# Optimization experiments

Measured on AMD Instinct MI355X. Metric: run time of the kernel, lower is better.

## Reference

```python
import jax, jax.numpy as jnp
import numpy as np
jax.config.update("jax_enable_x64", True)

TAPS, DELAY = 5, 3
EPS = 1e-6        # DNN_WPE.eps: power clamp before WPE
WPE_EPS = 1e-10   # wpe_one_iteration eps: inverse-power clamp + diag loading


def _signal_framing(Y, L):
    # Y: (..., T) -> (..., T-L+1, L) sliding frames (as_strided equivalent)
    T = Y.shape[-1]
    idx = jnp.arange(T - L + 1)[:, None] + jnp.arange(L)[None, :]
    return Y[..., idx]


def _wpe_one_iteration(Y, power, taps, delay):
    # Y: (B,F,C,T) complex128, power: (B,F,T) float64
    B, F, C, T = Y.shape
    inv_power = 1.0 / jnp.maximum(power, WPE_EPS)
    Tp = T - delay - taps + 1
    # tap-stacked delayed signal, taps axis reversed: (B,F,C,Tp,taps)
    Psi = _signal_framing(Y, taps)[..., :Tp, :][..., ::-1]
    Psi_n = Psi.conj() * inv_power[:, :, None, delay + taps - 1:, None]
    # covariance R: (B,F,taps*C,taps*C); cross-corr P: (B,F,taps,C_e,C_d)
    R = jnp.einsum("bfdtk,bfetl->bfkdle", Psi_n, Psi).reshape(B, F, taps * C, taps * C)
    P = jnp.einsum("bfdtk,bfet->bfked", Psi_n, Y[..., delay + taps - 1:])
    # v: (B,F,C_e,taps*C_d); conj filter G = inv(R) @ v^T  (X = v @ inv(R)^T)
    v = P.transpose(0, 1, 3, 2, 4).reshape(B, F, C, taps * C)
    eye = jnp.eye(taps * C, dtype=R.dtype)
    tr = jnp.trace(R, axis1=-2, axis2=-1).real[..., None, None] / (taps * C)
    G = jnp.linalg.solve(R + WPE_EPS * tr * eye, v.transpose(0, 1, 3, 2))
    G = G.reshape(B, F, taps, C, C)  # (B,F,tau,d,e) conjugated filter matrix
    # reverb tail: sum over taps of filtered, delayed signal
    tail = jnp.zeros_like(Y)
    for tau in range(taps):  # taps=5, small fixed loop
        s = delay + tau
        contrib = jnp.einsum("bfde,bfdt->bfet", G[:, :, tau], Y[..., : T - s])
        tail = tail.at[..., s:].add(contrib)
    return Y - tail


def setup_inputs() -> dict:
    key = jax.random.key(0)
    k1, k2, k3 = jax.random.split(key, 3)
    B, T, C, F = 4, 512, 8, 257
    data_real = jax.random.normal(k1, (B, T, C, F), dtype=jnp.float32)
    data_imag = jax.random.normal(k2, (B, T, C, F), dtype=jnp.float32)
    ilens = jax.random.randint(k3, (B,), 256, T + 1)
    return {"data_real": data_real, "data_imag": data_imag, "ilens": ilens}


def reference(data_real, data_imag, ilens):
    # (B,T,C,F) -> (B,F,C,T)
    data = (data_real + 1j * data_imag).transpose(0, 3, 2, 1)
    # power averaged over channels, clamped (B,F,T)
    power = jnp.maximum(jnp.mean(data.real ** 2 + data.imag ** 2, axis=-2), EPS)
    enh = _wpe_one_iteration(data.astype(jnp.complex128), power.astype(jnp.float64), TAPS, DELAY)
    enh = enh.astype(jnp.complex64)
    T = enh.shape[-1]
    pad = (jnp.arange(T)[None, :] >= ilens[:, None])[:, None, None, :]  # (B,1,1,T)
    enh = jnp.where(pad, 0.0 + 0.0j, enh)
    enh = enh.transpose(0, 3, 2, 1)  # back to (B,T,C,F)
    return enh.real, enh.imag, power
```

## Files before the change

### kernel.cpp

```cpp
#include <hip/hip_runtime.h>
#include <hip/hip_fp16.h>

#define B_ 4
#define T_ 512
#define C_ 8
#define F_ 257
#define TAPS 5
#define DELAY 3
#define N_ 40
#define NA 48
#define TP 505
#define T0 7
#define BF (B_*F_)
#define BTCF ((size_t)B_*T_*C_*F_)
#define YSH 532
#define YPAD 8
#define ZSD 20

typedef _Float16 half8 __attribute__((ext_vector_type(8)));
typedef float floatx4 __attribute__((ext_vector_type(4)));
typedef uint32_t uint32x4 __attribute__((ext_vector_type(4)));

__device__ inline uint32_t h2mul(uint32_t a, uint32_t b) {
    __half2 r = __hmul2(__builtin_bit_cast(__half2, a), __builtin_bit_cast(__half2, b));
    return __builtin_bit_cast(uint32_t, r);
}
__device__ inline uint32_t packf16(float2 v) {
    __half2 h = __floats2half2_rn(v.x, v.y);
    return __builtin_bit_cast(uint32_t, h);
}
__device__ inline float2 unpackf16(uint32_t u) {
    __half2 h = __builtin_bit_cast(__half2, u);
    return make_float2(__low2float(h), __high2float(h));
}
__device__ inline half8 mkfrag(uint32_t a, uint32_t b, uint32_t c, uint32_t d) {
    uint32x4 v = {a, b, c, d};
    return __builtin_bit_cast(half8, v);
}
__device__ inline int rowoff(int i) {
    return i * 49 - ((i * (i - 1)) >> 1);
}

struct Frag { half8 X; half8 Y; };

__device__ inline Frag build2(const uint32_t* p, uint32_t sw0, uint32_t sw1,
                              uint32_t sw2, uint32_t sw3) {
    uint32_t q0 = p[0], q1 = p[1], q2 = p[2], q3 = p[3];
    uint32_t q4 = p[4], q5 = p[5], q6 = p[6], q7 = p[7];
    uint32_t x0 = __builtin_amdgcn_perm(q1, q0, 0x05040100);
    uint32_t y0 = __builtin_amdgcn_perm(q1, q0, 0x07060302);
    uint32_t x1 = __builtin_amdgcn_perm(q3, q2, 0x05040100);
    uint32_t y1 = __builtin_amdgcn_perm(q3, q2, 0x07060302);
    uint32_t x2 = __builtin_amdgcn_perm(q5, q4, 0x05040100);
    uint32_t y2 = __builtin_amdgcn_perm(q5, q4, 0x07060302);
    uint32_t x3 = __builtin_amdgcn_perm(q7, q6, 0x05040100);
    uint32_t y3 = __builtin_amdgcn_perm(q7, q6, 0x07060302);
    Frag f;
    f.X = mkfrag(h2mul(x0, sw0), h2mul(x1, sw1), h2mul(x2, sw2), h2mul(x3, sw3));
    f.Y = mkfrag(h2mul(y0, sw0), h2mul(y1, sw1), h2mul(y2, sw2), h2mul(y3, sw3));
    return f;
}
__device__ inline int zs_off(int j) {
    return (j < N_) ? (j & 7) * YSH + (YPAD + 4 - (j >> 3)) : (j - N_) * YSH + (YPAD + T0);
}

__global__ __launch_bounds__(256) void k_fused(const float* __restrict__ in_re,
                                               const float* __restrict__ in_im,
                                               const int* __restrict__ ilens,
                                               float* __restrict__ out_re,
                                               float* __restrict__ out_im,
                                               float* __restrict__ pow_out) {
    __shared__ uint32_t sYh[C_ * YSH];
    __shared__ __align__(16) uint32_t pool[3256];
    float* sPow = (float*)pool;
    float2* sGT = (float2*)pool;
    uint32_t* sw_pk = pool + 640;
    float2* sAugU = (float2*)(pool + 896);
    int tid = threadIdx.x;

    int bid = blockIdx.x;
    int xcd = bid & 7, slot = bid >> 3;
    int w = (xcd < 4) ? xcd * 129 + slot : 516 + (xcd - 4) * 128 + slot;
    int b = w / F_;
    int f = w - b * F_;
    int ilen = ilens[b];
    const float* pre = in_re + (size_t)b * T_ * C_ * F_ + f;
    const float* pim = in_im + (size_t)b * T_ * C_ * F_ + f;

    {
        int t0 = tid, t1 = tid + 256;
        float s0 = 0.f, s1 = 0.f;
#pragma unroll 4
        for (int c = 0; c < C_; ++c) {
            size_t a0 = ((size_t)t0 * C_ + c) * F_;
            size_t a1 = ((size_t)t1 * C_ + c) * F_;
            float xr0 = pre[a0], xi0 = pim[a0];
            float xr1 = pre[a1], xi1 = pim[a1];
            sYh[c * YSH + YPAD + t0] = packf16(make_float2(xr0, xi0));
            sYh[c * YSH + YPAD + t1] = packf16(make_float2(xr1, xi1));
            s0 += xr0 * xr0 + xi0 * xi0;
            s1 += xr1 * xr1 + xi1 * xi1;
        }
        if (tid < 20) {
            int z = (tid < 8) ? tid : (512 + tid);
#pragma unroll
            for (int c = 0; c < C_; ++c) sYh[c * YSH + z] = 0;
        }
        s0 = fmaxf(s0 * (1.0f / C_), 1e-6f);
        s1 = fmaxf(s1 * (1.0f / C_), 1e-6f);
        pow_out[(size_t)w * T_ + t0] = s0;
        pow_out[(size_t)w * T_ + t1] = s1;
        sPow[t0] = s0;
        sPow[t1] = s1;
    }
    __syncthreads();

    {
        int k0 = 2 * tid, k1 = k0 + 1;
        float w0 = (k0 < TP) ? rsqrtf(sPow[k0 + T0]) : 0.f;
        float w1 = (k1 < TP) ? rsqrtf(sPow[k1 + T0]) : 0.f;
        sw_pk[tid] = packf16(make_float2(w0, w1));
    }
    __syncthreads();

    int wv = tid >> 6, ln = tid & 63;
    int kg = ln >> 4;
    if (wv < 3) {
        int r16 = ln & 15;
        int offB = zs_off(wv * 16 + r16);
#pragma unroll 1
        for (int mt = 0; mt < 3; ++mt) {
            int offA = zs_off(mt * 16 + r16);
            floatx4 aRe = {0.f, 0.f, 0.f, 0.f};
            floatx4 aIm = {0.f, 0.f, 0.f, 0.f};
#pragma unroll 2
            for (int ks = 0; ks < 16; ++ks) {
                int kbase = ks * 32 + kg * 8;
                uint32x4 sv = *(const uint32x4*)&sw_pk[kbase >> 1];
                Frag B = build2(&sYh[offB + kbase], sv[0], sv[1], sv[2], sv[3]);
                Frag A = build2(&sYh[offA + kbase], sv[0], sv[1], sv[2], sv[3]);
                half8 nYa = -A.Y;
                aRe = __builtin_amdgcn_mfma_f32_16x16x32_f16(A.X, B.X, aRe, 0, 0, 0);
                aRe = __builtin_amdgcn_mfma_f32_16x16x32_f16(A.Y, B.Y, aRe, 0, 0, 0);
                aIm = __builtin_amdgcn_mfma_f32_16x16x32_f16(A.X, B.Y, aIm, 0, 0, 0);
                aIm = __builtin_amdgcn_mfma_f32_16x16x32_f16(nYa, B.X, aIm, 0, 0, 0);
            }
#pragma unroll
            for (int r = 0; r < 4; ++r) {
                int m = mt * 16 + kg * 4 + r;
                int col = wv * 16 + r16;
                if (m < N_ && col >= m)
                    sAugU[rowoff(m) + col - m] = make_float2(aRe[r], aIm[r]);
            }
        }
    }
    __syncthreads();

    if (tid < 64) {
        float dv = (tid < N_) ? sAugU[rowoff(tid)].x : 0.f;
#pragma unroll
        for (int off = 32; off; off >>= 1) dv += __shfl_xor(dv, off, 64);
        if (tid < N_) sAugU[rowoff(tid)].x += 1e-10f * dv / N_;
    }
    __syncthreads();

    {
        int ri = tid >> 4, ci = tid & 15;
        float2 dq0, dq1, dq2;
#pragma unroll 1
        for (int p = 0; p < N_ - 2; p += 2) {
            if (p > 0 && ri == 0) {
                int qm = p - 1, roqm = rowoff(qm);
                if (ci < NA - qm)      sAugU[roqm + ci] = dq0;
                if (ci + 16 < NA - qm) sAugU[roqm + ci + 16] = dq1;
                if (ci + 32 < NA - qm) sAugU[roqm + ci + 32] = dq2;
            }
            int q = p + 1;
            int rop = rowoff(p), roq = rowoff(q);
            float2 Upp = sAugU[rop];
            float2 Upq = sAugU[rop + 1];
            float2 Uqq = sAugU[roq];
            float dn0 = Upp.x * Upp.x + Upp.y * Upp.y;
            float i0x = Upp.x / dn0, i0y = -Upp.y / dn0;
            float mqx = Upq.x * i0x + Upq.y * i0y;
            float mqy = Upq.x * i0y - Upq.y * i0x;
            float d1x = Uqq.x - (mqx * Upq.x - mqy * Upq.y);
            float d1y = Uqq.y - (mqx * Upq.y + mqy * Upq.x);
            float dn1 = d1x * d1x + d1y * d1y;
            float i1x = d1x / dn1, i1y = -d1y / dn1;
#pragma unroll 1
            for (int i = q + ri; i < N_; i += 16) {
                if (i == q) {
#pragma unroll
                    for (int s = 0; s < 3; ++s) {
                        int j = q + ci + 16 * s;
                        float2 r = make_float2(0.f, 0.f);
                        if (j < NA) {
                            float2 Upj = sAugU[rop + j - p];
                            float2 Uqj = sAugU[roq + j - q];
                            r.x = Uqj.x - (mqx * Upj.x - mqy * Upj.y);
                            r.y = Uqj.y - (mqx * Upj.y + mqy * Upj.x);
                        }
                        if (s == 0) dq0 = r; else if (s == 1) dq1 = r; else dq2 = r;
                    }
                } else {
                    float2 Upi = sAugU[rop + i - p];
                    float m0x = Upi.x * i0x + Upi.y * i0y;
                    float m0y = Upi.x * i0y - Upi.y * i0x;
                    float2 Uqi = sAugU[roq + i - q];
                    float ax = Uqi.x - (m0x * Upq.x - m0y * Upq.y);
                    float ay = -Uqi.y - (m0x * Upq.y + m0y * Upq.x);
                    float m1x = ax * i1x - ay * i1y;
                    float m1y = ax * i1y + ay * i1x;
                    int roi = rowoff(i) - i;
#pragma unroll 1
                    for (int j = i + ci; j < NA; j += 16) {
                        float2 Upj = sAugU[rop + j - p];
                        float2 Uqj = sAugU[roq + j - q];
                        float u1x = Uqj.x - (mqx * Upj.x - mqy * Upj.y);
                        float u1y = Uqj.y - (mqx * Upj.y + mqy * Upj.x);
                        float2 v = sAugU[roi + j];
                        v.x -= (m0x * Upj.x - m0y * Upj.y) + (m1x * u1x - m1y * u1y);
                        v.y -= (m0x * Upj.y + m0y * Upj.x) + (m1x * u1y + m1y * u1x);
                        sAugU[roi + j] = v;
                    }
                }
            }
            __syncthreads();
        }
        {
            int p = N_ - 2;
            if (ri == 0) {
                int qm = p - 1, roqm = rowoff(qm);
                if (ci < NA - qm)      sAugU[roqm + ci] = dq0;
                if (ci + 16 < NA - qm) sAugU[roqm + ci + 16] = dq1;
                if (ci + 32 < NA - qm) sAugU[roqm + ci + 32] = dq2;
            }
            int rop = rowoff(p);
            float2 piv = sAugU[rop];
            float dn = piv.x * piv.x + piv.y * piv.y;
            float px = piv.x / dn, py = -piv.y / dn;
#pragma unroll 1
            for (int i = p + 1 + ri; i < N_; i += 16) {
                float2 api = sAugU[rop + i - p];
                float mx = api.x * px + api.y * py;
                float my = api.x * py - api.y * px;
                int roi = rowoff(i) - i;
#pragma unroll 1
                for (int j = i + ci; j < NA; j += 16) {
                    float2 apj = sAugU[rop + j - p];
                    float2 v = sAugU[roi + j];
                    v.x -= mx * apj.x - my * apj.y;
                    v.y -= mx * apj.y + my * apj.x;
                    sAugU[roi + j] = v;
                }
            }
            __syncthreads();
        }
    }
    {
        int bc = tid & 7, br = tid >> 3;
        float2 defv = make_float2(0.f, 0.f);
        int defRow = -1;
#pragma unroll 1
        for (int p = N_ - 1; p >= 3; p -= 2) {
            if (defRow >= 0 && br == (defRow & 31))
                sAugU[rowoff(defRow) + N_ + bc - defRow] = defv;
            int q = p - 1;
            int rop = rowoff(p), roq = rowoff(q);
            float2 pivP = sAugU[rop];
            float dnP = pivP.x * pivP.x + pivP.y * pivP.y;
            float pPx = pivP.x / dnP, pPy = -pivP.y / dnP;
            float2 rhsP = sAugU[rop + N_ + bc - p];
            float xPx = rhsP.x * pPx - rhsP.y * pPy;
            float xPy = rhsP.x * pPy + rhsP.y * pPx;
            float2 pivQ = sAugU[roq];
            float dnQ = pivQ.x * pivQ.x + pivQ.y * pivQ.y;
            float pQx = pivQ.x / dnQ, pQy = -pivQ.y / dnQ;
            float2 Uqp = sAugU[roq + 1];
            float2 rhsQ = sAugU[roq + N_ + bc - q];
            float rqx = rhsQ.x - (Uqp.x * xPx - Uqp.y * xPy);
            float rqy = rhsQ.y - (Uqp.x * xPy + Uqp.y * xPx);
            float xQx = rqx * pQx - rqy * pQy;
            float xQy = rqx * pQy + rqy * pQx;
#pragma unroll 1
            for (int i = br; i <= p - 2; i += 32) {
                int roi = rowoff(i) - i;
                float2 Uip = sAugU[roi + p];
                float2 Uiq = sAugU[roi + q];
                float2 v = sAugU[roi + N_ + bc];
                v.x -= (Uip.x * xPx - Uip.y * xPy) + (Uiq.x * xQx - Uiq.y * xQy);
                v.y -= (Uip.x * xPy + Uip.y * xPx) + (Uiq.x * xQy + Uiq.y * xQx);
                sAugU[roi + N_ + bc] = v;
            }
            if (br == (q & 31)) defv = make_float2(rqx, rqy);
            defRow = q;
            __syncthreads();
        }
        {
            if (defRow >= 0 && br == (defRow & 31))
                sAugU[rowoff(defRow) + N_ + bc - defRow] = defv;
            int rop = rowoff(1);
            float2 piv = sAugU[rop];
            float dn = piv.x * piv.x + piv.y * piv.y;
            float px = piv.x / dn, py = -piv.y / dn;
            float2 rhs = sAugU[rop + N_ + bc - 1];
            float xr = rhs.x * px - rhs.y * py;
            float xi = rhs.x * py + rhs.y * px;
            if (br == 0) {
                float2 aip = sAugU[1];
                float2 v = sAugU[N_ + bc];
                v.x -= aip.x * xr - aip.y * xi;
                v.y -= aip.x * xi + aip.y * xr;
                sAugU[N_ + bc] = v;
            }
            __syncthreads();
        }
    }
    for (int idx = tid; idx < N_ * C_; idx += 256) {
        int j = idx >> 3;
        int e = idx & 7;
        int roj = rowoff(j);
        float2 piv = sAugU[roj];
        float dnm = piv.x * piv.x + piv.y * piv.y;
        float pix = piv.x / dnm, piy = -piv.y / dnm;
        float2 rhs = sAugU[roj + N_ + e - j];
        int tau = j >> 3, d = j & 7;
        sGT[(e * C_ + d) * TAPS + tau] =
            make_float2(rhs.x * pix - rhs.y * piy, rhs.x * piy + rhs.y * pix);
    }
    __syncthreads();

    half8 aFr[2], aFi[2];
    {
        int m = ln & 15;
#pragma unroll
        for (int ks = 0; ks < 2; ++ks) {
            half8 hr = {}, hi = {};
#pragma unroll
            for (int q = 0; q < 8; ++q) {
                int j = ks * 32 + kg * 8 + q;
                float gx = 0.f, gy = 0.f;
                if (m < 8 && j < N_) {
                    float2 g = sGT[(m * C_ + (j & 7)) * TAPS + (j >> 3)];
                    gx = g.x; gy = g.y;
                }
                hr[q] = (_Float16)gx;
                hi[q] = (_Float16)gy;
            }
            aFr[ks] = hr;
            aFi[ks] = hi;
        }
    }
    __syncthreads();

    uint32_t* zRe = pool;
    uint32_t* zIm = pool + 64 * ZSD;
    int trow = wv * 16 + (ln & 15);
#pragma unroll 1
    for (int ch = 0; ch < 8; ++ch) {
        int c0 = ch * 64;
        for (int idx = tid; idx < 1280; idx += 256) {
            int jp = idx >> 6, tl = idx & 63;
            int j0 = 2 * jp, j1 = j0 + 1;
            int base = c0 + tl + (YPAD - 3);
            uint32_t y0 = sYh[(j0 & 7) * YSH + base - (j0 >> 3)];
            uint32_t y1 = sYh[(j1 & 7) * YSH + base - (j1 >> 3)];
            zRe[tl * ZSD + jp] = __builtin_amdgcn_perm(y1, y0, 0x05040100);
            zIm[tl * ZSD + jp] = __builtin_amdgcn_perm(y1, y0, 0x07060302);
        }
        __syncthreads();
        floatx4 accR = {0.f, 0.f, 0.f, 0.f};
        floatx4 accI = {0.f, 0.f, 0.f, 0.f};
        {
            int o0 = trow * ZSD + kg * 4;
            half8 Br0 = __builtin_bit_cast(half8, *(const uint32x4*)&zRe[o0]);
            half8 Bi0 = __builtin_bit_cast(half8, *(const uint32x4*)&zIm[o0]);
            half8 Br1 = {}, Bi1 = {};
            if (kg == 0) {
                int o1 = trow * ZSD + 16;
                Br1 = __builtin_bit_cast(half8, *(const uint32x4*)&zRe[o1]);
                Bi1 = __builtin_bit_cast(half8, *(const uint32x4*)&zIm[o1]);
            }
            half8 nFi0 = -aFi[0], nFi1 = -aFi[1];
            accR = __builtin_amdgcn_mfma_f32_16x16x32_f16(aFr[0], Br0, accR, 0, 0, 0);
            accR = __builtin_amdgcn_mfma_f32_16x16x32_f16(aFr[1], Br1, accR, 0, 0, 0);
            accI = __builtin_amdgcn_mfma_f32_16x16x32_f16(aFi[0], Br0, accI, 0, 0, 0);
            accI = __builtin_amdgcn_mfma_f32_16x16x32_f16(aFi[1], Br1, accI, 0, 0, 0);
            accR = __builtin_amdgcn_mfma_f32_16x16x32_f16(nFi0, Bi0, accR, 0, 0, 0);
            accR = __builtin_amdgcn_mfma_f32_16x16x32_f16(nFi1, Bi1, accR, 0, 0, 0);
            accI = __builtin_amdgcn_mfma_f32_16x16x32_f16(aFr[0], Bi0, accI, 0, 0, 0);
            accI = __builtin_amdgcn_mfma_f32_16x16x32_f16(aFr[1], Bi1, accI, 0, 0, 0);
        }
        if (kg < 2) {
            int tg = c0 + trow;
            bool dead = (tg >= ilen);
#pragma unroll
            for (int r = 0; r < 4; ++r) {
                int e = kg * 4 + r;
                float2 cf = unpackf16(sYh[e * YSH + YPAD + tg]);
                float ex = cf.x - accR[r];
                float ey = cf.y - accI[r];
                if (dead) { ex = 0.f; ey = 0.f; }
                size_t o = (size_t)b * T_ * C_ * F_ + ((size_t)tg * C_ + e) * F_ + f;
                out_re[o] = ex;
                out_im[o] = ey;
            }
        }
        __syncthreads();
    }
}

extern "C" void kernel_launch(void* const* d_in, const int* in_sizes, int n_in,
                              void* d_out, int out_size, void* d_ws, size_t ws_size,
                              hipStream_t stream) {
    const float* in_re = (const float*)d_in[0];
    const float* in_im = (const float*)d_in[1];
    const int* ilens = (const int*)d_in[2];

    float* out_re = (float*)d_out;
    float* out_im = out_re + BTCF;
    float* out_pw = out_im + BTCF;

    k_fused<<<BF, 256, 0, stream>>>(in_re, in_im, ilens, out_re, out_im, out_pw);
}
```

Measured before the change: 188.3 us.

## Raise block to 384 threads and give each wave one Gram-matrix tile

Raises the block size from 256 to 384 threads so six waves each compute one upper-triangular 16x16 tile of the covariance via MFMA, instead of three waves looping over three row tiles. Diagonal tiles reuse the B fragment as A, which removes a redundant fragment build. The elimination row loops now stride by 24 rows, and the filter is solved in place in the augmented matrix, dropping the separate transposed filter buffer. The aim is more parallelism in the Gram and solve phases, at the cost of more threads per block, which may lower occupancy, and two idle waves in the output stage.

```diff
diff --git a/kernel.cpp b/kernel.cpp
--- a/kernel.cpp
+++ b/kernel.cpp
@@ -16,6 +16,7 @@
 #define YSH 532
 #define YPAD 8
 #define ZSD 20
+#define NTHR 384
 
 typedef _Float16 half8 __attribute__((ext_vector_type(8)));
 typedef float floatx4 __attribute__((ext_vector_type(4)));
@@ -64,16 +65,15 @@
     return (j < N_) ? (j & 7) * YSH + (YPAD + 4 - (j >> 3)) : (j - N_) * YSH + (YPAD + T0);
 }
 
-__global__ __launch_bounds__(256) void k_fused(const float* __restrict__ in_re,
-                                               const float* __restrict__ in_im,
-                                               const int* __restrict__ ilens,
-                                               float* __restrict__ out_re,
-                                               float* __restrict__ out_im,
-                                               float* __restrict__ pow_out) {
+__global__ __launch_bounds__(NTHR) void k_fused(const float* __restrict__ in_re,
+                                                const float* __restrict__ in_im,
+                                                const int* __restrict__ ilens,
+                                                float* __restrict__ out_re,
+                                                float* __restrict__ out_im,
+                                                float* __restrict__ pow_out) {
     __shared__ uint32_t sYh[C_ * YSH];
     __shared__ __align__(16) uint32_t pool[3256];
     float* sPow = (float*)pool;
-    float2* sGT = (float2*)pool;
     uint32_t* sw_pk = pool + 640;
     float2* sAugU = (float2*)(pool + 896);
     int tid = threadIdx.x;
@@ -88,34 +88,29 @@
     const float* pim = in_im + (size_t)b * T_ * C_ * F_ + f;
 
     {
-        int t0 = tid, t1 = tid + 256;
-        float s0 = 0.f, s1 = 0.f;
+#pragma unroll 1
+        for (int t = tid; t < T_; t += NTHR) {
+            float sacc = 0.f;
 #pragma unroll 4
-        for (int c = 0; c < C_; ++c) {
-            size_t a0 = ((size_t)t0 * C_ + c) * F_;
-            size_t a1 = ((size_t)t1 * C_ + c) * F_;
-            float xr0 = pre[a0], xi0 = pim[a0];
-            float xr1 = pre[a1], xi1 = pim[a1];
-            sYh[c * YSH + YPAD + t0] = packf16(make_float2(xr0, xi0));
-            sYh[c * YSH + YPAD + t1] = packf16(make_float2(xr1, xi1));
-            s0 += xr0 * xr0 + xi0 * xi0;
-            s1 += xr1 * xr1 + xi1 * xi1;
+            for (int c = 0; c < C_; ++c) {
+                size_t a = ((size_t)t * C_ + c) * F_;
+                float xr = pre[a], xi = pim[a];
+                sYh[c * YSH + YPAD + t] = packf16(make_float2(xr, xi));
+                sacc += xr * xr + xi * xi;
+            }
+            sacc = fmaxf(sacc * (1.0f / C_), 1e-6f);
+            pow_out[(size_t)w * T_ + t] = sacc;
+            sPow[t] = sacc;
         }
         if (tid < 20) {
             int z = (tid < 8) ? tid : (512 + tid);
 #pragma unroll
             for (int c = 0; c < C_; ++c) sYh[c * YSH + z] = 0;
         }
-        s0 = fmaxf(s0 * (1.0f / C_), 1e-6f);
-        s1 = fmaxf(s1 * (1.0f / C_), 1e-6f);
-        pow_out[(size_t)w * T_ + t0] = s0;
-        pow_out[(size_t)w * T_ + t1] = s1;
-        sPow[t0] = s0;
-        sPow[t1] = s1;
-    }
-    __syncthreads();
-
-    {
+    }
+    __syncthreads();
+
+    if (tid < 256) {
         int k0 = 2 * tid, k1 = k0 + 1;
         float w0 = (k0 < TP) ? rsqrtf(sPow[k0 + T0]) : 0.f;
         float w1 = (k1 < TP) ? rsqrtf(sPow[k1 + T0]) : 0.f;
@@ -123,35 +118,37 @@
     }
     __syncthreads();
 
-    int wv = tid >> 6, ln = tid & 63;
+    int wv = tid / 64, ln = tid & 63;
     int kg = ln >> 4;
-    if (wv < 3) {
+    {
         int r16 = ln & 15;
-        int offB = zs_off(wv * 16 + r16);
-#pragma unroll 1
-        for (int mt = 0; mt < 3; ++mt) {
-            int offA = zs_off(mt * 16 + r16);
-            floatx4 aRe = {0.f, 0.f, 0.f, 0.f};
-            floatx4 aIm = {0.f, 0.f, 0.f, 0.f};
+        int mt = (wv < 3) ? 0 : ((wv < 5) ? 1 : 2);
+        int nt = (wv < 3) ? wv : ((wv < 5) ? wv - 2 : 2);
+        bool diag = (mt == nt);
+        int offB = zs_off(nt * 16 + r16);
+        int offA = zs_off(mt * 16 + r16);
+        floatx4 aRe = {0.f, 0.f, 0.f, 0.f};
+        floatx4 aIm = {0.f, 0.f, 0.f, 0.f};
 #pragma unroll 2
-            for (int ks = 0; ks < 16; ++ks) {
-                int kbase = ks * 32 + kg * 8;
-                uint32x4 sv = *(const uint32x4*)&sw_pk[kbase >> 1];
-                Frag B = build2(&sYh[offB + kbase], sv[0], sv[1], sv[2], sv[3]);
-                Frag A = build2(&sYh[offA + kbase], sv[0], sv[1], sv[2], sv[3]);
-                half8 nYa = -A.Y;
-                aRe = __builtin_amdgcn_mfma_f32_16x16x32_f16(A.X, B.X, aRe, 0, 0, 0);
-                aRe = __builtin_amdgcn_mfma_f32_16x16x32_f16(A.Y, B.Y, aRe, 0, 0, 0);
-                aIm = __builtin_amdgcn_mfma_f32_16x16x32_f16(A.X, B.Y, aIm, 0, 0, 0);
-                aIm = __builtin_amdgcn_mfma_f32_16x16x32_f16(nYa, B.X, aIm, 0, 0, 0);
-            }
-#pragma unroll
-            for (int r = 0; r < 4; ++r) {
-                int m = mt * 16 + kg * 4 + r;
-                int col = wv * 16 + r16;
-                if (m < N_ && col >= m)
-                    sAugU[rowoff(m) + col - m] = make_float2(aRe[r], aIm[r]);
-            }
+        for (int ks = 0; ks < 16; ++ks) {
+            int kbase = ks * 32 + kg * 8;
+            uint32x4 sv = *(const uint32x4*)&sw_pk[kbase >> 1];
+            Frag B = build2(&sYh[offB + kbase], sv[0], sv[1], sv[2], sv[3]);
+            Frag A;
+            if (diag) A = B;
+            else A = build2(&sYh[offA + kbase], sv[0], sv[1], sv[2], sv[3]);
+            half8 nYa = -A.Y;
+            aRe = __builtin_amdgcn_mfma_f32_16x16x32_f16(A.X, B.X, aRe, 0, 0, 0);
+            aRe = __builtin_amdgcn_mfma_f32_16x16x32_f16(A.Y, B.Y, aRe, 0, 0, 0);
+            aIm = __builtin_amdgcn_mfma_f32_16x16x32_f16(A.X, B.Y, aIm, 0, 0, 0);
+            aIm = __builtin_amdgcn_mfma_f32_16x16x32_f16(nYa, B.X, aIm, 0, 0, 0);
+        }
+        int col = nt * 16 + r16;
+#pragma unroll
+        for (int r = 0; r < 4; ++r) {
+            int m = mt * 16 + kg * 4 + r;
+            if (m < N_ && col >= m)
+                sAugU[rowoff(m) + col - m] = make_float2(aRe[r], aIm[r]);
         }
     }
     __syncthreads();
@@ -189,7 +186,7 @@
             float dn1 = d1x * d1x + d1y * d1y;
             float i1x = d1x / dn1, i1y = -d1y / dn1;
 #pragma unroll 1
-            for (int i = q + ri; i < N_; i += 16) {
+            for (int i = q + ri; i < N_; i += 24) {
                 if (i == q) {
 #pragma unroll
                     for (int s = 0; s < 3; ++s) {
@@ -241,7 +238,7 @@
             float dn = piv.x * piv.x + piv.y * piv.y;
             float px = piv.x / dn, py = -piv.y / dn;
 #pragma unroll 1
-            for (int i = p + 1 + ri; i < N_; i += 16) {
+            for (int i = p + 1 + ri; i < N_; i += 24) {
                 float2 api = sAugU[rop + i - p];
                 float mx = api.x * px + api.y * py;
                 float my = api.x * py - api.y * px;
@@ -283,8 +280,8 @@
             float rqy = rhsQ.y - (Uqp.x * xPy + Uqp.y * xPx);
             float xQx = rqx * pQx - rqy * pQy;
             float xQy = rqx * pQy + rqy * pQx;
-#pragma unroll 1
-            for (int i = br; i <= p - 2; i += 32) {
+            if (br <= p - 2) {
+                int i = br;
                 int roi = rowoff(i) - i;
                 float2 Uip = sAugU[roi + p];
                 float2 Uiq = sAugU[roi + q];
@@ -317,22 +314,21 @@
             __syncthreads();
         }
     }
-    for (int idx = tid; idx < N_ * C_; idx += 256) {
-        int j = idx >> 3;
-        int e = idx & 7;
+    if (tid < N_ * C_) {
+        int j = tid >> 3;
+        int e = tid & 7;
         int roj = rowoff(j);
         float2 piv = sAugU[roj];
         float dnm = piv.x * piv.x + piv.y * piv.y;
         float pix = piv.x / dnm, piy = -piv.y / dnm;
         float2 rhs = sAugU[roj + N_ + e - j];
-        int tau = j >> 3, d = j & 7;
-        sGT[(e * C_ + d) * TAPS + tau] =
+        sAugU[roj + N_ + e - j] =
             make_float2(rhs.x * pix - rhs.y * piy, rhs.x * piy + rhs.y * pix);
     }
     __syncthreads();
 
-    half8 aFr[2], aFi[2];
-    {
+    half8 aFr[2] = {}, aFi[2] = {};
+    if (wv < 4) {
         int m = ln & 15;
 #pragma unroll
         for (int ks = 0; ks < 2; ++ks) {
@@ -342,7 +338,7 @@
                 int j = ks * 32 + kg * 8 + q;
                 float gx = 0.f, gy = 0.f;
                 if (m < 8 && j < N_) {
-                    float2 g = sGT[(m * C_ + (j & 7)) * TAPS + (j >> 3)];
+                    float2 g = sAugU[rowoff(j) + N_ + m - j];
                     gx = g.x; gy = g.y;
                 }
                 hr[q] = (_Float16)gx;
@@ -360,7 +356,7 @@
 #pragma unroll 1
     for (int ch = 0; ch < 8; ++ch) {
         int c0 = ch * 64;
-        for (int idx = tid; idx < 1280; idx += 256) {
+        for (int idx = tid; idx < 1280; idx += NTHR) {
             int jp = idx >> 6, tl = idx & 63;
             int j0 = 2 * jp, j1 = j0 + 1;
             int base = c0 + tl + (YPAD - 3);
@@ -370,41 +366,43 @@
             zIm[tl * ZSD + jp] = __builtin_amdgcn_perm(y1, y0, 0x07060302);
         }
         __syncthreads();
-        floatx4 accR = {0.f, 0.f, 0.f, 0.f};
-        floatx4 accI = {0.f, 0.f, 0.f, 0.f};
-        {
-            int o0 = trow * ZSD + kg * 4;
-            half8 Br0 = __builtin_bit_cast(half8, *(const uint32x4*)&zRe[o0]);
-            half8 Bi0 = __builtin_bit_cast(half8, *(const uint32x4*)&zIm[o0]);
-            half8 Br1 = {}, Bi1 = {};
-            if (kg == 0) {
-                int o1 = trow * ZSD + 16;
-                Br1 = __builtin_bit_cast(half8, *(const uint32x4*)&zRe[o1]);
-                Bi1 = __builtin_bit_cast(half8, *(const uint32x4*)&zIm[o1]);
-            }
-            half8 nFi0 = -aFi[0], nFi1 = -aFi[1];
-            accR = __builtin_amdgcn_mfma_f32_16x16x32_f16(aFr[0], Br0, accR, 0, 0, 0);
-            accR = __builtin_amdgcn_mfma_f32_16x16x32_f16(aFr[1], Br1, accR, 0, 0, 0);
-            accI = __builtin_amdgcn_mfma_f32_16x16x32_f16(aFi[0], Br0, accI, 0, 0, 0);
-            accI = __builtin_amdgcn_mfma_f32_16x16x32_f16(aFi[1], Br1, accI, 0, 0, 0);
-            accR = __builtin_amdgcn_mfma_f32_16x16x32_f16(nFi0, Bi0, accR, 0, 0, 0);
-            accR = __builtin_amdgcn_mfma_f32_16x16x32_f16(nFi1, Bi1, accR, 0, 0, 0);
-            accI = __builtin_amdgcn_mfma_f32_16x16x32_f16(aFr[0], Bi0, accI, 0, 0, 0);
-            accI = __builtin_amdgcn_mfma_f32_16x16x32_f16(aFr[1], Bi1, accI, 0, 0, 0);
-        }
-        if (kg < 2) {
-            int tg = c0 + trow;
-            bool dead = (tg >= ilen);
-#pragma unroll
-            for (int r = 0; r < 4; ++r) {
-                int e = kg * 4 + r;
-                float2 cf = unpackf16(sYh[e * YSH + YPAD + tg]);
-                float ex = cf.x - accR[r];
-                float ey = cf.y - accI[r];
-                if (dead) { ex = 0.f; ey = 0.f; }
-                size_t o = (size_t)b * T_ * C_ * F_ + ((size_t)tg * C_ + e) * F_ + f;
-                out_re[o] = ex;
-                out_im[o] = ey;
+        if (wv < 4) {
+            floatx4 accR = {0.f, 0.f, 0.f, 0.f};
+            floatx4 accI = {0.f, 0.f, 0.f, 0.f};
+            {
+                int o0 = trow * ZSD + kg * 4;
+                half8 Br0 = __builtin_bit_cast(half8, *(const uint32x4*)&zRe[o0]);
+                half8 Bi0 = __builtin_bit_cast(half8, *(const uint32x4*)&zIm[o0]);
+                half8 Br1 = {}, Bi1 = {};
+                if (kg == 0) {
+                    int o1 = trow * ZSD + 16;
+                    Br1 = __builtin_bit_cast(half8, *(const uint32x4*)&zRe[o1]);
+                    Bi1 = __builtin_bit_cast(half8, *(const uint32x4*)&zIm[o1]);
+                }
+                half8 nFi0 = -aFi[0], nFi1 = -aFi[1];
+                accR = __builtin_amdgcn_mfma_f32_16x16x32_f16(aFr[0], Br0, accR, 0, 0, 0);
+                accR = __builtin_amdgcn_mfma_f32_16x16x32_f16(aFr[1], Br1, accR, 0, 0, 0);
+                accI = __builtin_amdgcn_mfma_f32_16x16x32_f16(aFi[0], Br0, accI, 0, 0, 0);
+                accI = __builtin_amdgcn_mfma_f32_16x16x32_f16(aFi[1], Br1, accI, 0, 0, 0);
+                accR = __builtin_amdgcn_mfma_f32_16x16x32_f16(nFi0, Bi0, accR, 0, 0, 0);
+                accR = __builtin_amdgcn_mfma_f32_16x16x32_f16(nFi1, Bi1, accR, 0, 0, 0);
+                accI = __builtin_amdgcn_mfma_f32_16x16x32_f16(aFr[0], Bi0, accI, 0, 0, 0);
+                accI = __builtin_amdgcn_mfma_f32_16x16x32_f16(aFr[1], Bi1, accI, 0, 0, 0);
+            }
+            if (kg < 2) {
+                int tg = c0 + trow;
+                bool dead = (tg >= ilen);
+#pragma unroll
+                for (int r = 0; r < 4; ++r) {
+                    int e = kg * 4 + r;
+                    float2 cf = unpackf16(sYh[e * YSH + YPAD + tg]);
+                    float ex = cf.x - accR[r];
+                    float ey = cf.y - accI[r];
+                    if (dead) { ex = 0.f; ey = 0.f; }
+                    size_t o = (size_t)b * T_ * C_ * F_ + ((size_t)tg * C_ + e) * F_ + f;
+                    out_re[o] = ex;
+                    out_im[o] = ey;
+                }
             }
         }
         __syncthreads();
@@ -422,5 +420,5 @@
     float* out_im = out_re + BTCF;
     float* out_pw = out_im + BTCF;
 
-    k_fused<<<BF, 256, 0, stream>>>(in_re, in_im, ilens, out_re, out_im, out_pw);
-}
+    k_fused<<<BF, NTHR, 0, stream>>>(in_re, in_im, ilens, out_re, out_im, out_pw);
+}
```

Measured after the change: 193.9 us. 1.03x slower.

## Split input staging into separate kernel writing packed fp16 workspace

Applied to the files above, without the earlier changes.

Adds a staging kernel that reads the strided fp32 input, packs each sample to half2, computes the channel power, and writes a contiguous per-(b,f) buffer to workspace. The main kernel then loads that buffer with contiguous reads instead of stride-F gathers. The solved filter is written back into the augmented matrix in place rather than into a separate transposed array. The aim is to avoid the poorly coalesced gather inside the long-running fused kernel, at the cost of an extra launch and a workspace write and read.

```diff
diff --git a/kernel.cpp b/kernel.cpp
--- a/kernel.cpp
+++ b/kernel.cpp
@@ -39,6 +39,10 @@
 }
 __device__ inline int rowoff(int i) {
     return i * 49 - ((i * (i - 1)) >> 1);
+}
+__device__ inline int swz_w(int bid) {
+    int xcd = bid & 7, slot = bid >> 3;
+    return (xcd < 4) ? xcd * 129 + slot : 516 + (xcd - 4) * 128 + slot;
 }
 
 struct Frag { half8 X; half8 Y; };
@@ -64,54 +68,70 @@
     return (j < N_) ? (j & 7) * YSH + (YPAD + 4 - (j >> 3)) : (j - N_) * YSH + (YPAD + T0);
 }
 
-__global__ __launch_bounds__(256) void k_fused(const float* __restrict__ in_re,
+__global__ __launch_bounds__(256) void k_stage(const float* __restrict__ in_re,
                                                const float* __restrict__ in_im,
+                                               uint32_t* __restrict__ Yh,
+                                               float* __restrict__ pow_out) {
+    int w = swz_w(blockIdx.x);
+    int b = w / F_;
+    int f = w - b * F_;
+    const float* pre = in_re + (size_t)b * T_ * C_ * F_ + f;
+    const float* pim = in_im + (size_t)b * T_ * C_ * F_ + f;
+    int t = blockIdx.y * 256 + threadIdx.x;
+    float s = 0.f;
+    uint32_t pk0, pk1, pk2, pk3, pk4, pk5, pk6, pk7;
+#pragma unroll
+    for (int c = 0; c < C_; ++c) {
+        size_t a = ((size_t)t * C_ + c) * F_;
+        float xr = pre[a], xi = pim[a];
+        uint32_t pk = packf16(make_float2(xr, xi));
+        s += xr * xr + xi * xi;
+        switch (c) {
+            case 0: pk0 = pk; break; case 1: pk1 = pk; break;
+            case 2: pk2 = pk; break; case 3: pk3 = pk; break;
+            case 4: pk4 = pk; break; case 5: pk5 = pk; break;
+            case 6: pk6 = pk; break; default: pk7 = pk; break;
+        }
+    }
+    uint32_t* yw = Yh + (size_t)w * (C_ * T_) + t;
+    yw[0 * T_] = pk0; yw[1 * T_] = pk1; yw[2 * T_] = pk2; yw[3 * T_] = pk3;
+    yw[4 * T_] = pk4; yw[5 * T_] = pk5; yw[6 * T_] = pk6; yw[7 * T_] = pk7;
+    pow_out[(size_t)w * T_ + t] = fmaxf(s * (1.0f / C_), 1e-6f);
+}
+
+__global__ __launch_bounds__(256) void k_fused(const uint32_t* __restrict__ Yh,
+                                               const float* __restrict__ pow_in,
                                                const int* __restrict__ ilens,
                                                float* __restrict__ out_re,
-                                               float* __restrict__ out_im,
-                                               float* __restrict__ pow_out) {
+                                               float* __restrict__ out_im) {
     __shared__ uint32_t sYh[C_ * YSH];
     __shared__ __align__(16) uint32_t pool[3256];
     float* sPow = (float*)pool;
-    float2* sGT = (float2*)pool;
     uint32_t* sw_pk = pool + 640;
     float2* sAugU = (float2*)(pool + 896);
     int tid = threadIdx.x;
 
-    int bid = blockIdx.x;
-    int xcd = bid & 7, slot = bid >> 3;
-    int w = (xcd < 4) ? xcd * 129 + slot : 516 + (xcd - 4) * 128 + slot;
+    int w = swz_w(blockIdx.x);
     int b = w / F_;
     int f = w - b * F_;
     int ilen = ilens[b];
-    const float* pre = in_re + (size_t)b * T_ * C_ * F_ + f;
-    const float* pim = in_im + (size_t)b * T_ * C_ * F_ + f;
 
     {
-        int t0 = tid, t1 = tid + 256;
-        float s0 = 0.f, s1 = 0.f;
+        const uint32_t* ys = Yh + (size_t)w * (C_ * T_);
 #pragma unroll 4
-        for (int c = 0; c < C_; ++c) {
-            size_t a0 = ((size_t)t0 * C_ + c) * F_;
-            size_t a1 = ((size_t)t1 * C_ + c) * F_;
-            float xr0 = pre[a0], xi0 = pim[a0];
-            float xr1 = pre[a1], xi1 = pim[a1];
-            sYh[c * YSH + YPAD + t0] = packf16(make_float2(xr0, xi0));
-            sYh[c * YSH + YPAD + t1] = packf16(make_float2(xr1, xi1));
-            s0 += xr0 * xr0 + xi0 * xi0;
-            s1 += xr1 * xr1 + xi1 * xi1;
+        for (int k = 0; k < 16; ++k) {
+            int idx = tid + k * 256;
+            int c = idx >> 9, t = idx & 511;
+            sYh[c * YSH + YPAD + t] = ys[idx];
         }
         if (tid < 20) {
             int z = (tid < 8) ? tid : (512 + tid);
 #pragma unroll
             for (int c = 0; c < C_; ++c) sYh[c * YSH + z] = 0;
         }
-        s0 = fmaxf(s0 * (1.0f / C_), 1e-6f);
-        s1 = fmaxf(s1 * (1.0f / C_), 1e-6f);
-        pow_out[(size_t)w * T_ + t0] = s0;
-        pow_out[(size_t)w * T_ + t1] = s1;
-        sPow[t0] = s0;
-        sPow[t1] = s1;
+        const float* pw = pow_in + (size_t)w * T_;
+        sPow[tid] = pw[tid];
+        sPow[tid + 256] = pw[tid + 256];
     }
     __syncthreads();
 
@@ -325,8 +345,7 @@
         float dnm = piv.x * piv.x + piv.y * piv.y;
         float pix = piv.x / dnm, piy = -piv.y / dnm;
         float2 rhs = sAugU[roj + N_ + e - j];
-        int tau = j >> 3, d = j & 7;
-        sGT[(e * C_ + d) * TAPS + tau] =
+        sAugU[roj + N_ + e - j] =
             make_float2(rhs.x * pix - rhs.y * piy, rhs.x * piy + rhs.y * pix);
     }
     __syncthreads();
@@ -342,7 +361,7 @@
                 int j = ks * 32 + kg * 8 + q;
                 float gx = 0.f, gy = 0.f;
                 if (m < 8 && j < N_) {
-                    float2 g = sGT[(m * C_ + (j & 7)) * TAPS + (j >> 3)];
+                    float2 g = sAugU[rowoff(j) + N_ + m - j];
                     gx = g.x; gy = g.y;
                 }
                 hr[q] = (_Float16)gx;
@@ -422,5 +441,8 @@
     float* out_im = out_re + BTCF;
     float* out_pw = out_im + BTCF;
 
-    k_fused<<<BF, 256, 0, stream>>>(in_re, in_im, ilens, out_re, out_im, out_pw);
-}
+    uint32_t* Yh = (uint32_t*)d_ws;
+
+    k_stage<<<dim3(BF, 2), 256, 0, stream>>>(in_re, in_im, Yh, out_pw);
+    k_fused<<<BF, 256, 0, stream>>>(Yh, out_pw, ilens, out_re, out_im);
+}
```

Measured after the change: 209.7 us. 11.4% more time.

## Split fused WPE kernel into staging transpose, gram-solve, and tail kernels

Applied to the files above, without the earlier changes.

Adds a staging kernel that transposes the (B,T,C,F) float input into a packed fp16 (B,F,C,T) workspace through a shared-memory tile, so each frequency's data becomes contiguous and later loads coalesce instead of striding by F. The gram/solve kernel then reads the staged data and writes the filter to a global buffer. A separate tail kernel applies the filter, split over two time halves to double the number of blocks. The cost is two extra launches and a global round trip for the staged signal and filter. The tail also now reads the signal straight from global memory instead of shared memory.

```diff
diff --git a/kernel.cpp b/kernel.cpp
--- a/kernel.cpp
+++ b/kernel.cpp
@@ -39,6 +39,10 @@
 }
 __device__ inline int rowoff(int i) {
     return i * 49 - ((i * (i - 1)) >> 1);
+}
+__device__ inline int swz_w(int bid) {
+    int xcd = bid & 7, slot = bid >> 3;
+    return (xcd < 4) ? xcd * 129 + slot : 516 + (xcd - 4) * 128 + slot;
 }
 
 struct Frag { half8 X; half8 Y; };
@@ -64,47 +68,71 @@
     return (j < N_) ? (j & 7) * YSH + (YPAD + 4 - (j >> 3)) : (j - N_) * YSH + (YPAD + T0);
 }
 
-__global__ __launch_bounds__(256) void k_fused(const float* __restrict__ in_re,
+__global__ __launch_bounds__(256) void k_stage(const float* __restrict__ in_re,
                                                const float* __restrict__ in_im,
-                                               const int* __restrict__ ilens,
-                                               float* __restrict__ out_re,
-                                               float* __restrict__ out_im,
-                                               float* __restrict__ pow_out) {
+                                               uint32_t* __restrict__ Yh) {
+    __shared__ uint32_t tile[32][33];
+    int ft = blockIdx.x % 9;
+    int tt = blockIdx.x / 9;
+    int c = blockIdx.y, b = blockIdx.z;
+    int tx = threadIdx.x, ty = threadIdx.y;
+    int f = ft * 32 + tx;
+#pragma unroll
+    for (int i = 0; i < 4; ++i) {
+        int t = tt * 32 + ty + i * 8;
+        if (f < F_) {
+            size_t idx = ((size_t)(b * T_ + t) * C_ + c) * F_ + f;
+            tile[ty + i * 8][tx] = packf16(make_float2(in_re[idx], in_im[idx]));
+        }
+    }
+    __syncthreads();
+    int t2 = tt * 32 + tx;
+#pragma unroll
+    for (int i = 0; i < 4; ++i) {
+        int f2 = ft * 32 + ty + i * 8;
+        if (f2 < F_) {
+            Yh[((size_t)(b * F_ + f2) * C_ + c) * T_ + t2] = tile[tx][ty + i * 8];
+        }
+    }
+}
+
+__global__ __launch_bounds__(256) void k_gramsolve(const uint32_t* __restrict__ Yh,
+                                                   float2* __restrict__ Gbuf,
+                                                   float* __restrict__ pow_out) {
     __shared__ uint32_t sYh[C_ * YSH];
     __shared__ __align__(16) uint32_t pool[3256];
     float* sPow = (float*)pool;
-    float2* sGT = (float2*)pool;
     uint32_t* sw_pk = pool + 640;
     float2* sAugU = (float2*)(pool + 896);
     int tid = threadIdx.x;
 
-    int bid = blockIdx.x;
-    int xcd = bid & 7, slot = bid >> 3;
-    int w = (xcd < 4) ? xcd * 129 + slot : 516 + (xcd - 4) * 128 + slot;
-    int b = w / F_;
-    int f = w - b * F_;
-    int ilen = ilens[b];
-    const float* pre = in_re + (size_t)b * T_ * C_ * F_ + f;
-    const float* pim = in_im + (size_t)b * T_ * C_ * F_ + f;
+    int w = swz_w(blockIdx.x);
+
+    {
+        const uint32_t* ys = Yh + (size_t)w * (C_ * T_);
+#pragma unroll 4
+        for (int k = 0; k < 16; ++k) {
+            int idx = tid + k * 256;
+            int c = idx >> 9, t = idx & 511;
+            sYh[c * YSH + YPAD + t] = ys[idx];
+        }
+        if (tid < 20) {
+            int z = (tid < 8) ? tid : (512 + tid);
+#pragma unroll
+            for (int c = 0; c < C_; ++c) sYh[c * YSH + z] = 0;
+        }
+    }
+    __syncthreads();
 
     {
         int t0 = tid, t1 = tid + 256;
         float s0 = 0.f, s1 = 0.f;
-#pragma unroll 4
+#pragma unroll
         for (int c = 0; c < C_; ++c) {
-            size_t a0 = ((size_t)t0 * C_ + c) * F_;
-            size_t a1 = ((size_t)t1 * C_ + c) * F_;
-            float xr0 = pre[a0], xi0 = pim[a0];
-            float xr1 = pre[a1], xi1 = pim[a1];
-            sYh[c * YSH + YPAD + t0] = packf16(make_float2(xr0, xi0));
-            sYh[c * YSH + YPAD + t1] = packf16(make_float2(xr1, xi1));
-            s0 += xr0 * xr0 + xi0 * xi0;
-            s1 += xr1 * xr1 + xi1 * xi1;
-        }
-        if (tid < 20) {
-            int z = (tid < 8) ? tid : (512 + tid);
-#pragma unroll
-            for (int c = 0; c < C_; ++c) sYh[c * YSH + z] = 0;
+            float2 a0 = unpackf16(sYh[c * YSH + YPAD + t0]);
+            float2 a1 = unpackf16(sYh[c * YSH + YPAD + t1]);
+            s0 += a0.x * a0.x + a0.y * a0.y;
+            s1 += a1.x * a1.x + a1.y * a1.y;
         }
         s0 = fmaxf(s0 * (1.0f / C_), 1e-6f);
         s1 = fmaxf(s1 * (1.0f / C_), 1e-6f);
@@ -325,11 +353,27 @@
         float dnm = piv.x * piv.x + piv.y * piv.y;
         float pix = piv.x / dnm, piy = -piv.y / dnm;
         float2 rhs = sAugU[roj + N_ + e - j];
-        int tau = j >> 3, d = j & 7;
-        sGT[(e * C_ + d) * TAPS + tau] =
+        Gbuf[(size_t)w * (N_ * C_) + idx] =
             make_float2(rhs.x * pix - rhs.y * piy, rhs.x * piy + rhs.y * pix);
     }
-    __syncthreads();
+}
+
+__global__ __launch_bounds__(256) void k_tail(const uint32_t* __restrict__ Yh,
+                                              const float2* __restrict__ Gbuf,
+                                              const int* __restrict__ ilens,
+                                              float* __restrict__ out_re,
+                                              float* __restrict__ out_im) {
+    __shared__ __align__(16) uint32_t zRe[64 * ZSD];
+    __shared__ __align__(16) uint32_t zIm[64 * ZSD];
+    int w = swz_w(blockIdx.x);
+    int half = blockIdx.y;
+    int b = w / F_;
+    int f = w - b * F_;
+    int ilen = ilens[b];
+    const uint32_t* yw = Yh + (size_t)w * (C_ * T_);
+    const float2* gw = Gbuf + (size_t)w * (N_ * C_);
+    int tid = threadIdx.x;
+    int wv = tid >> 6, ln = tid & 63, kg = ln >> 4;
 
     half8 aFr[2], aFi[2];
     {
@@ -342,7 +386,7 @@
                 int j = ks * 32 + kg * 8 + q;
                 float gx = 0.f, gy = 0.f;
                 if (m < 8 && j < N_) {
-                    float2 g = sGT[(m * C_ + (j & 7)) * TAPS + (j >> 3)];
+                    float2 g = gw[j * 8 + m];
                     gx = g.x; gy = g.y;
                 }
                 hr[q] = (_Float16)gx;
@@ -352,20 +396,20 @@
             aFi[ks] = hi;
         }
     }
-    __syncthreads();
-
-    uint32_t* zRe = pool;
-    uint32_t* zIm = pool + 64 * ZSD;
+
     int trow = wv * 16 + (ln & 15);
 #pragma unroll 1
-    for (int ch = 0; ch < 8; ++ch) {
-        int c0 = ch * 64;
+    for (int ch = 0; ch < 4; ++ch) {
+        int c0 = half * 256 + ch * 64;
         for (int idx = tid; idx < 1280; idx += 256) {
             int jp = idx >> 6, tl = idx & 63;
             int j0 = 2 * jp, j1 = j0 + 1;
-            int base = c0 + tl + (YPAD - 3);
-            uint32_t y0 = sYh[(j0 & 7) * YSH + base - (j0 >> 3)];
-            uint32_t y1 = sYh[(j1 & 7) * YSH + base - (j1 >> 3)];
+            int s0 = c0 + tl - 3 - (j0 >> 3);
+            uint32_t y0 = 0, y1 = 0;
+            if (s0 >= 0) {
+                y0 = yw[(j0 & 7) * T_ + s0];
+                y1 = yw[(j1 & 7) * T_ + s0];
+            }
             zRe[tl * ZSD + jp] = __builtin_amdgcn_perm(y1, y0, 0x05040100);
             zIm[tl * ZSD + jp] = __builtin_amdgcn_perm(y1, y0, 0x07060302);
         }
@@ -398,7 +442,7 @@
 #pragma unroll
             for (int r = 0; r < 4; ++r) {
                 int e = kg * 4 + r;
-                float2 cf = unpackf16(sYh[e * YSH + YPAD + tg]);
+                float2 cf = unpackf16(yw[e * T_ + tg]);
                 float ex = cf.x - accR[r];
                 float ey = cf.y - accI[r];
                 if (dead) { ex = 0.f; ey = 0.f; }
@@ -422,5 +466,12 @@
     float* out_im = out_re + BTCF;
     float* out_pw = out_im + BTCF;
 
-    k_fused<<<BF, 256, 0, stream>>>(in_re, in_im, ilens, out_re, out_im, out_pw);
-}
+    uint32_t* Yh = (uint32_t*)d_ws;
+    float2* Gbuf = (float2*)(Yh + (size_t)BF * C_ * T_);
+
+    dim3 tb(32, 8);
+    dim3 tg(9 * 16, C_, B_);
+    k_stage<<<tg, tb, 0, stream>>>(in_re, in_im, Yh);
+    k_gramsolve<<<BF, 256, 0, stream>>>(Yh, Gbuf, out_pw);
+    k_tail<<<dim3(BF, 2), 256, 0, stream>>>(Yh, Gbuf, ilens, out_re, out_im);
+}
```

Result: slower. 221.1 us (+17.5%).
